# Kernel tuning notes

Hardware: AMD Instinct MI355X
Metric: run time of the kernel (lower is better)

## Reference

```python
import jax, jax.numpy as jnp
import numpy as np

KD, KH, KW = 3, 3, 3
C = 64

def setup_inputs() -> dict:
    key = jax.random.key(0)
    kx, kw = jax.random.split(key)
    x = jax.random.normal(kx, (4, 16, 112, 112, C), dtype=jnp.float32)
    # One 3x3x3 filter per channel; DHWIO layout with I=in_per_group=1, O=C
    w = jax.random.normal(kw, (KD, KH, KW, 1, C), dtype=jnp.float32) * 0.1
    return {"x": x, "w": w}

def reference(x, w) -> jnp.ndarray:
    # Depthwise 3D conv: feature_group_count=C makes each output channel the
    # conv of the matching input channel with its own [3,3,3] kernel, which is
    # exactly the per-channel Conv3D(filters=1) loop + concat in the original.
    return jax.lax.conv_general_dilated(
        x, w,
        window_strides=(1, 1, 1),
        padding="SAME",
        dimension_numbers=("NDHWC", "DHWIO", "NDHWC"),
        feature_group_count=C,
    )
```

## Files before the change

kernel.cpp:

```cpp
#include <hip/hip_runtime.h>

#define N_ 4
#define D_ 16
#define H_ 112
#define W_ 112
#define C_ 64

#define DO_ 2
#define HO_ 2
#define DT_ (D_ / DO_)
#define HTILES (H_ / HO_)
#define WAVES_PER_BLOCK 4
#define HGROUPS (HTILES / WAVES_PER_BLOCK)
#define WSPLIT 2
#define WHALF (W_ / WSPLIT)

__global__ __launch_bounds__(256)
void dwconv3d_kernel(const float* __restrict__ x,
                     const float* __restrict__ wgt,
                     float* __restrict__ out) {
    int b = blockIdx.x;
    const int wh = b % WSPLIT; b /= WSPLIT;
    const int hg = b % HGROUPS; b /= HGROUPS;
    const int dt = b % DT_;     b /= DT_;
    const int n  = b;

    const int lane = threadIdx.x & 63;
    const int wid  = threadIdx.x >> 6;
    const int c    = lane;

    const int d0 = dt * DO_;
    const int h0 = (hg * WAVES_PER_BLOCK + wid) * HO_;
    const int w0 = wh * WHALF;

    float wt[3][3][3];
#pragma unroll
    for (int kd = 0; kd < 3; ++kd)
#pragma unroll
      for (int kh = 0; kh < 3; ++kh)
#pragma unroll
        for (int kw = 0; kw < 3; ++kw)
          wt[kd][kh][kw] = wgt[((kd * 3 + kh) * 3 + kw) * C_ + c];

    const float* px[4][4];
    float msk[4][4];
#pragma unroll
    for (int dr = 0; dr < 4; ++dr) {
      int d = d0 - 1 + dr;
      bool dv = (d >= 0) && (d < D_);
      int dc = d < 0 ? 0 : (d > D_ - 1 ? D_ - 1 : d);
#pragma unroll
      for (int hr = 0; hr < 4; ++hr) {
        int h = h0 - 1 + hr;
        bool hv = (h >= 0) && (h < H_);
        int hc = h < 0 ? 0 : (h > H_ - 1 ? H_ - 1 : h);
        msk[dr][hr] = (dv && hv) ? 1.0f : 0.0f;
        px[dr][hr] = x + (size_t)((n * D_ + dc) * H_ + hc) * W_ * C_ + c;
      }
    }

    float win[3][4][4];

    if (w0 == 0) {
#pragma unroll
      for (int dr = 0; dr < 4; ++dr)
#pragma unroll
        for (int hr = 0; hr < 4; ++hr)
          win[0][dr][hr] = 0.0f;
    } else {
#pragma unroll
      for (int dr = 0; dr < 4; ++dr)
#pragma unroll
        for (int hr = 0; hr < 4; ++hr)
          win[0][dr][hr] = msk[dr][hr] * px[dr][hr][(size_t)(w0 - 1) * C_];
    }
#pragma unroll
    for (int dr = 0; dr < 4; ++dr)
#pragma unroll
      for (int hr = 0; hr < 4; ++hr) {
        win[1][dr][hr] = msk[dr][hr] * px[dr][hr][(size_t)(w0)     * C_];
        win[2][dr][hr] = msk[dr][hr] * px[dr][hr][(size_t)(w0 + 1) * C_];
      }

    float* po[2][2];
#pragma unroll
    for (int od = 0; od < 2; ++od)
#pragma unroll
      for (int oh = 0; oh < 2; ++oh)
        po[od][oh] = out + ((size_t)((n * D_ + d0 + od) * H_ + (h0 + oh)) * W_ + w0) * C_ + c;

#pragma unroll
    for (int dr = 0; dr < 4; ++dr)
#pragma unroll
      for (int hr = 0; hr < 4; ++hr)
        px[dr][hr] += (size_t)(w0 + 2) * C_;

#pragma unroll 4
    for (int w = w0; w < w0 + WHALF; ++w) {
      float acc[2][2];
#pragma unroll
      for (int od = 0; od < 2; ++od)
#pragma unroll
        for (int oh = 0; oh < 2; ++oh) {
          float a = 0.0f;
#pragma unroll
          for (int kw = 0; kw < 3; ++kw)
#pragma unroll
            for (int kd = 0; kd < 3; ++kd)
#pragma unroll
              for (int kh = 0; kh < 3; ++kh)
                a += win[kw][od + kd][oh + kh] * wt[kd][kh][kw];
          acc[od][oh] = a;
        }
#pragma unroll
      for (int od = 0; od < 2; ++od)
#pragma unroll
        for (int oh = 0; oh < 2; ++oh) {
          *po[od][oh] = acc[od][oh];
          po[od][oh] += C_;
        }
#pragma unroll
      for (int dr = 0; dr < 4; ++dr)
#pragma unroll
        for (int hr = 0; hr < 4; ++hr) {
          win[0][dr][hr] = win[1][dr][hr];
          win[1][dr][hr] = win[2][dr][hr];
        }
      if (w + 2 < W_) {
#pragma unroll
        for (int dr = 0; dr < 4; ++dr)
#pragma unroll
          for (int hr = 0; hr < 4; ++hr) {
            win[2][dr][hr] = msk[dr][hr] * px[dr][hr][0];
            px[dr][hr] += C_;
          }
      } else {
#pragma unroll
        for (int dr = 0; dr < 4; ++dr)
#pragma unroll
          for (int hr = 0; hr < 4; ++hr)
            win[2][dr][hr] = 0.0f;
      }
    }
}

extern "C" void kernel_launch(void* const* d_in, const int* in_sizes, int n_in,
                              void* d_out, int out_size, void* d_ws, size_t ws_size,
                              hipStream_t stream) {
    const float* x   = (const float*)d_in[0];
    const float* wgt = (const float*)d_in[1];
    float* out = (float*)d_out;

    dim3 grid(N_ * DT_ * HGROUPS * WSPLIT);
    dim3 block(256);
    dwconv3d_kernel<<<grid, block, 0, stream>>>(x, wgt, out);
}
```

Measured before the change: 387.3 us.

## Use zero-page halo pointers, prefetch next column, widen W split, swizzle blocks

Out-of-range d/h rows now point at a zeroed device buffer, which removes the per-load mask multiplies. Each row keeps one shared byte offset, so address arithmetic shrinks to scalar bases plus a single vector offset. The next W column is loaded before the FMA block, overlapping load latency with compute, and the loop is reordered so all four accumulators update together. The W split goes from 2 to 4 for more blocks, launch bounds ask for 4 blocks per CU, and block IDs are swizzled across groups of 8. The zpage global is never written, so it relies on device globals being zero-initialised.

Result: faster. 372.9 us (-3.7%).

```diff
diff --git a/kernel.cpp b/kernel.cpp
--- a/kernel.cpp
+++ b/kernel.cpp
@@ -12,26 +12,30 @@
 #define HTILES (H_ / HO_)
 #define WAVES_PER_BLOCK 4
 #define HGROUPS (HTILES / WAVES_PER_BLOCK)
-#define WSPLIT 2
-#define WHALF (W_ / WSPLIT)
+#define WSPLIT 4
+#define WQ (W_ / WSPLIT)
+#define NWG (N_ * DT_ * HGROUPS * WSPLIT)
+#define CB (C_ * 4)
 
-__global__ __launch_bounds__(256)
+__device__ float zpage[W_ * C_];
+
+__global__ __launch_bounds__(256, 4)
 void dwconv3d_kernel(const float* __restrict__ x,
                      const float* __restrict__ wgt,
                      float* __restrict__ out) {
     int b = blockIdx.x;
+    b = (b & 7) * (NWG / 8) + (b >> 3);
     const int wh = b % WSPLIT; b /= WSPLIT;
     const int hg = b % HGROUPS; b /= HGROUPS;
     const int dt = b % DT_;     b /= DT_;
     const int n  = b;
 
-    const int lane = threadIdx.x & 63;
-    const int wid  = threadIdx.x >> 6;
-    const int c    = lane;
+    const int c   = threadIdx.x & 63;
+    const int wid = __builtin_amdgcn_readfirstlane(threadIdx.x >> 6);
 
     const int d0 = dt * DO_;
     const int h0 = (hg * WAVES_PER_BLOCK + wid) * HO_;
-    const int w0 = wh * WHALF;
+    const int w0 = wh * WQ;
 
     float wt[3][3][3];
 #pragma unroll
@@ -42,105 +46,92 @@
         for (int kw = 0; kw < 3; ++kw)
           wt[kd][kh][kw] = wgt[((kd * 3 + kh) * 3 + kw) * C_ + c];
 
-    const float* px[4][4];
-    float msk[4][4];
+    const char* bx[4][4];
 #pragma unroll
     for (int dr = 0; dr < 4; ++dr) {
-      int d = d0 - 1 + dr;
-      bool dv = (d >= 0) && (d < D_);
-      int dc = d < 0 ? 0 : (d > D_ - 1 ? D_ - 1 : d);
+      const int d = d0 - 1 + dr;
 #pragma unroll
       for (int hr = 0; hr < 4; ++hr) {
-        int h = h0 - 1 + hr;
-        bool hv = (h >= 0) && (h < H_);
-        int hc = h < 0 ? 0 : (h > H_ - 1 ? H_ - 1 : h);
-        msk[dr][hr] = (dv && hv) ? 1.0f : 0.0f;
-        px[dr][hr] = x + (size_t)((n * D_ + dc) * H_ + hc) * W_ * C_ + c;
+        const int h = h0 - 1 + hr;
+        if (d >= 0 && d < D_ && h >= 0 && h < H_)
+          bx[dr][hr] = (const char*)(x + (size_t)((n * D_ + d) * H_ + h) * W_ * C_);
+        else
+          bx[dr][hr] = (const char*)zpage;
       }
     }
 
+    char* ox[2][2];
+#pragma unroll
+    for (int od = 0; od < 2; ++od)
+#pragma unroll
+      for (int oh = 0; oh < 2; ++oh)
+        ox[od][oh] = (char*)(out +
+            (size_t)((n * D_ + d0 + od) * H_ + (h0 + oh)) * W_ * C_);
+
+    unsigned vb = (unsigned)((w0 + 2) * CB) + (unsigned)(c * 4);
+
     float win[3][4][4];
-
-    if (w0 == 0) {
+#pragma unroll
+    for (int dr = 0; dr < 4; ++dr)
+#pragma unroll
+      for (int hr = 0; hr < 4; ++hr) {
+        win[1][dr][hr] = *(const float*)(bx[dr][hr] + (vb - 2 * CB));
+        win[2][dr][hr] = *(const float*)(bx[dr][hr] + (vb - 1 * CB));
+        win[0][dr][hr] = 0.0f;
+      }
+    if (w0 != 0) {
 #pragma unroll
       for (int dr = 0; dr < 4; ++dr)
 #pragma unroll
         for (int hr = 0; hr < 4; ++hr)
-          win[0][dr][hr] = 0.0f;
-    } else {
+          win[0][dr][hr] = *(const float*)(bx[dr][hr] + (vb - 3 * CB));
+    }
+
+#pragma unroll 4
+    for (int w = w0; w < w0 + WQ; ++w) {
+      float nxt[4][4];
+      if (w + 2 < W_) {
 #pragma unroll
-      for (int dr = 0; dr < 4; ++dr)
+        for (int dr = 0; dr < 4; ++dr)
 #pragma unroll
-        for (int hr = 0; hr < 4; ++hr)
-          win[0][dr][hr] = msk[dr][hr] * px[dr][hr][(size_t)(w0 - 1) * C_];
-    }
+          for (int hr = 0; hr < 4; ++hr)
+            nxt[dr][hr] = *(const float*)(bx[dr][hr] + vb);
+      } else {
 #pragma unroll
-    for (int dr = 0; dr < 4; ++dr)
+        for (int dr = 0; dr < 4; ++dr)
 #pragma unroll
-      for (int hr = 0; hr < 4; ++hr) {
-        win[1][dr][hr] = msk[dr][hr] * px[dr][hr][(size_t)(w0)     * C_];
-        win[2][dr][hr] = msk[dr][hr] * px[dr][hr][(size_t)(w0 + 1) * C_];
+          for (int hr = 0; hr < 4; ++hr)
+            nxt[dr][hr] = 0.0f;
       }
 
-    float* po[2][2];
+      float acc[2][2] = {{0.0f, 0.0f}, {0.0f, 0.0f}};
 #pragma unroll
-    for (int od = 0; od < 2; ++od)
+      for (int kw = 0; kw < 3; ++kw)
 #pragma unroll
-      for (int oh = 0; oh < 2; ++oh)
-        po[od][oh] = out + ((size_t)((n * D_ + d0 + od) * H_ + (h0 + oh)) * W_ + w0) * C_ + c;
+        for (int kd = 0; kd < 3; ++kd)
+#pragma unroll
+          for (int kh = 0; kh < 3; ++kh)
+#pragma unroll
+            for (int od = 0; od < 2; ++od)
+#pragma unroll
+              for (int oh = 0; oh < 2; ++oh)
+                acc[od][oh] += win[kw][od + kd][oh + kh] * wt[kd][kh][kw];
 
-#pragma unroll
-    for (int dr = 0; dr < 4; ++dr)
-#pragma unroll
-      for (int hr = 0; hr < 4; ++hr)
-        px[dr][hr] += (size_t)(w0 + 2) * C_;
-
-#pragma unroll 4
-    for (int w = w0; w < w0 + WHALF; ++w) {
-      float acc[2][2];
 #pragma unroll
       for (int od = 0; od < 2; ++od)
 #pragma unroll
-        for (int oh = 0; oh < 2; ++oh) {
-          float a = 0.0f;
-#pragma unroll
-          for (int kw = 0; kw < 3; ++kw)
-#pragma unroll
-            for (int kd = 0; kd < 3; ++kd)
-#pragma unroll
-              for (int kh = 0; kh < 3; ++kh)
-                a += win[kw][od + kd][oh + kh] * wt[kd][kh][kw];
-          acc[od][oh] = a;
-        }
-#pragma unroll
-      for (int od = 0; od < 2; ++od)
-#pragma unroll
-        for (int oh = 0; oh < 2; ++oh) {
-          *po[od][oh] = acc[od][oh];
-          po[od][oh] += C_;
-        }
+        for (int oh = 0; oh < 2; ++oh)
+          *(float*)(ox[od][oh] + (vb - 2 * CB)) = acc[od][oh];
+
 #pragma unroll
       for (int dr = 0; dr < 4; ++dr)
 #pragma unroll
         for (int hr = 0; hr < 4; ++hr) {
           win[0][dr][hr] = win[1][dr][hr];
           win[1][dr][hr] = win[2][dr][hr];
+          win[2][dr][hr] = nxt[dr][hr];
         }
-      if (w + 2 < W_) {
-#pragma unroll
-        for (int dr = 0; dr < 4; ++dr)
-#pragma unroll
-          for (int hr = 0; hr < 4; ++hr) {
-            win[2][dr][hr] = msk[dr][hr] * px[dr][hr][0];
-            px[dr][hr] += C_;
-          }
-      } else {
-#pragma unroll
-        for (int dr = 0; dr < 4; ++dr)
-#pragma unroll
-          for (int hr = 0; hr < 4; ++hr)
-            win[2][dr][hr] = 0.0f;
-      }
+      vb += CB;
     }
 }
 
@@ -151,7 +142,7 @@
     const float* wgt = (const float*)d_in[1];
     float* out = (float*)d_out;
 
-    dim3 grid(N_ * DT_ * HGROUPS * WSPLIT);
+    dim3 grid(NWG);
     dim3 block(256);
     dwconv3d_kernel<<<grid, block, 0, stream>>>(x, wgt, out);
 }
```
